# Performance work log

Hardware: AMD Instinct MI355X
Metric: run time of the kernel (lower is better)

## Reference

```python
import jax, jax.numpy as jnp
import numpy as np

B, C, H, W = 8, 64, 128, 128
EPS = 1e-5


def setup_inputs() -> dict:
    key = jax.random.key(0)
    ks = jax.random.split(key, 12)
    d = {
        'x_1': jax.random.normal(ks[0], (B, C, H, W), jnp.float32),
        'x_cur': jax.random.normal(ks[1], (B, C, H, W), jnp.float32),
        # 1x1 conv projections (stored as [out_c, in_c])
        'Wq': jax.random.normal(ks[2], (C, C), jnp.float32) * (1.0 / np.sqrt(C)),
        'bq': jnp.zeros((C,), jnp.float32),
        'Wk': jax.random.normal(ks[3], (C, C), jnp.float32) * (1.0 / np.sqrt(C)),
        'bk': jnp.zeros((C,), jnp.float32),
        'Wv': jax.random.normal(ks[4], (C, C), jnp.float32) * (1.0 / np.sqrt(C)),
        'bv': jnp.zeros((C,), jnp.float32),
        'gamma': jnp.ones((1,), jnp.float32),
        # conv_cur: 3x3 conv (no bias) + BN + ReLU, then 1x1 conv (no bias) + BN + ReLU
        'conv1_w': jax.random.normal(ks[5], (C, C, 3, 3), jnp.float32) * (1.0 / np.sqrt(9 * C)),
        'bn1_scale': jnp.ones((C,), jnp.float32),
        'bn1_bias': jnp.zeros((C,), jnp.float32),
        'bn1_mean': jax.random.normal(ks[6], (C,), jnp.float32) * 0.1,
        'bn1_var': jax.random.uniform(ks[7], (C,), jnp.float32, 0.5, 1.5),
        'conv2_w': jax.random.normal(ks[8], (C, C, 1, 1), jnp.float32) * (1.0 / np.sqrt(C)),
        'bn2_scale': jnp.ones((C,), jnp.float32),
        'bn2_bias': jnp.zeros((C,), jnp.float32),
        'bn2_mean': jax.random.normal(ks[9], (C,), jnp.float32) * 0.1,
        'bn2_var': jax.random.uniform(ks[10], (C,), jnp.float32, 0.5, 1.5),
    }
    return d


def _conv1x1(x, w, b):
    # x: [B,C,H,W], w: [O,C] -> [B,O,H,W]
    return jnp.einsum('oc,bchw->bohw', w, x) + b[None, :, None, None]


def _bn_relu(x, scale, bias, mean, var):
    inv = scale / jnp.sqrt(var + EPS)
    return jax.nn.relu(x * inv[None, :, None, None] + (bias - mean * inv)[None, :, None, None])


def reference(x_1, x_cur, Wq, bq, Wk, bk, Wv, bv, gamma, conv1_w,
              bn1_scale, bn1_bias, bn1_mean, bn1_var, conv2_w,
              bn2_scale, bn2_bias, bn2_mean, bn2_var):
    q = _conv1x1(x_1, Wq, bq)          # [B,C,H,W]
    k = _conv1x1(x_cur, Wk, bk)        # [B,C,H,W]
    v = _conv1x1(x_cur, Wv, bv)        # [B,C,H,W]
    # energy[b,c,w,w'] = sum_h q[b,c,h,w] * k[b,c,h,w']  (Q transposed on H/W)
    energy = jnp.einsum('bchw,bchv->bcwv', q, k)          # [B,C,W,W]
    attention = jax.nn.softmax(energy, axis=2)             # softmax over dim 2
    out = jnp.einsum('bchw,bcwv->bchv', v, attention)      # [B,C,H,W]
    y = gamma * out + x_cur
    # 3x3 conv + BN + ReLU (dropout is identity in eval)
    y = jax.lax.conv_general_dilated(y, conv1_w, (1, 1), 'SAME',
                                     dimension_numbers=('NCHW', 'OIHW', 'NCHW'))
    y = _bn_relu(y, bn1_scale, bn1_bias, bn1_mean, bn1_var)
    # 1x1 conv + BN + ReLU
    y = jnp.einsum('oc,bchw->bohw', conv2_w[:, :, 0, 0], y)
    y = _bn_relu(y, bn2_scale, bn2_bias, bn2_mean, bn2_var)
    return y
```

## Files before the change

kernel.cpp:

```cpp
#include <hip/hip_runtime.h>

#define HW    16384
#define CHW   1048576
#define EPSV  1e-5f
#define PITCH 68
#define APITCH 132

typedef short bf16x8 __attribute__((ext_vector_type(8)));
typedef float f32x4 __attribute__((ext_vector_type(4)));
typedef unsigned short u16x4 __attribute__((ext_vector_type(4)));

static __device__ __forceinline__ unsigned short f2b(float f) {
    union { float f; unsigned int i; } x; x.f = f;
    unsigned int i = x.i + 0x7fffu + ((x.i >> 16) & 1u);
    return (unsigned short)(i >> 16);
}

static __device__ __forceinline__ bf16x8 frag_load(const unsigned short* p) {
    union { u16x4 h[2]; bf16x8 v; } u;
    u.h[0] = *(const u16x4*)(p);
    u.h[1] = *(const u16x4*)(p + 4);
    return u.v;
}
static __device__ __forceinline__ bf16x8 gfrag(const unsigned short* p) {
    return *(const bf16x8*)p;
}
static __device__ __forceinline__ f32x4 mfma16(bf16x8 a, bf16x8 b, f32x4 c) {
    return __builtin_amdgcn_mfma_f32_16x16x32_bf16(a, b, c, 0, 0, 0);
}

__global__ void prep_kernel(const float* __restrict__ Wq, const float* __restrict__ Wk,
                            const float* __restrict__ Wv,
                            const float* __restrict__ c1w,
                            const float* __restrict__ bn1s, const float* __restrict__ bn1b,
                            const float* __restrict__ bn1m, const float* __restrict__ bn1v,
                            const float* __restrict__ c2w,
                            const float* __restrict__ bn2s, const float* __restrict__ bn2b,
                            const float* __restrict__ bn2m, const float* __restrict__ bn2v,
                            unsigned short* __restrict__ Wqb, unsigned short* __restrict__ Wkb,
                            unsigned short* __restrict__ Wvb, unsigned short* __restrict__ W3b,
                            unsigned short* __restrict__ W2b, float* __restrict__ beta1,
                            float* __restrict__ beta2)
{
    int i = blockIdx.x * blockDim.x + threadIdx.x;
    if (i < 12288) {
        int mat = i >> 12, r = i & 4095;
        const float* src = (mat == 0) ? Wq : ((mat == 1) ? Wk : Wv);
        unsigned short* dst = (mat == 0) ? Wqb : ((mat == 1) ? Wkb : Wvb);
        dst[r] = f2b(src[r]);
    } else if (i < 49152) {
        int j = i - 12288;
        int dydx = j >> 12, r = j & 4095, o = r >> 6, c = r & 63;
        float inv = bn1s[o] * rsqrtf(bn1v[o] + EPSV);
        W3b[j] = f2b(c1w[o * 576 + c * 9 + dydx] * inv);
    } else if (i < 53248) {
        int r = i - 49152, o = r >> 6;
        float inv = bn2s[o] * rsqrtf(bn2v[o] + EPSV);
        W2b[r] = f2b(c2w[r] * inv);
    } else if (i < 53376) {
        int j = i - 53248;
        if (j < 64) {
            float inv = bn1s[j] * rsqrtf(bn1v[j] + EPSV);
            beta1[j] = bn1b[j] - bn1m[j] * inv;
        } else {
            int o = j - 64;
            float inv = bn2s[o] * rsqrtf(bn2v[o] + EPSV);
            beta2[o] = bn2b[o] - bn2m[o] * inv;
        }
    }
}

__global__ __launch_bounds__(256) void qkv_kernel(
    const float* __restrict__ x1, const float* __restrict__ xc,
    const unsigned short* __restrict__ Wqb, const unsigned short* __restrict__ Wkb,
    const unsigned short* __restrict__ Wvb,
    const float* __restrict__ bq, const float* __restrict__ bk,
    const float* __restrict__ bv,
    unsigned short* __restrict__ qo, unsigned short* __restrict__ ko,
    unsigned short* __restrict__ vo)
{
    __shared__ __align__(16) unsigned short XT[2][128][PITCH];
    int t = threadIdx.x;
    int b = blockIdx.x >> 7;
    int p0 = (blockIdx.x & 127) << 7;

    const float* xs1 = x1 + b * CHW + p0;
    const float* xs2 = xc + b * CHW + p0;
    for (int idx = t; idx < 2048; idx += 256) {
        int c0 = ((idx >> 6) & 31) << 1, p2 = (idx & 63) << 1;
        float2 a0 = *(const float2*)&xs1[c0 * HW + p2];
        float2 a1 = *(const float2*)&xs1[(c0 + 1) * HW + p2];
        *(unsigned int*)&XT[0][p2][c0]     = f2b(a0.x) | ((unsigned int)f2b(a1.x) << 16);
        *(unsigned int*)&XT[0][p2 + 1][c0] = f2b(a0.y) | ((unsigned int)f2b(a1.y) << 16);
        float2 b0 = *(const float2*)&xs2[c0 * HW + p2];
        float2 b1 = *(const float2*)&xs2[(c0 + 1) * HW + p2];
        *(unsigned int*)&XT[1][p2][c0]     = f2b(b0.x) | ((unsigned int)f2b(b1.x) << 16);
        *(unsigned int*)&XT[1][p2 + 1][c0] = f2b(b0.y) | ((unsigned int)f2b(b1.y) << 16);
    }
    __syncthreads();

    int lane = t & 63, wid = t >> 6;
    int i16 = lane & 15;
    int g8 = (lane >> 4) << 3;
    int g4 = (lane >> 4) << 2;
    int n0 = wid << 5;

    bf16x8 bfr[2][2][2];
    #pragma unroll
    for (int inp = 0; inp < 2; ++inp)
        #pragma unroll
        for (int nt = 0; nt < 2; ++nt)
            #pragma unroll
            for (int ks = 0; ks < 2; ++ks)
                bfr[inp][nt][ks] = frag_load(&XT[inp][n0 + nt * 16 + i16][ks * 32 + g8]);

    f32x4 zz = {0.f, 0.f, 0.f, 0.f};
    f32x4 acc[3][4][2];
    #pragma unroll
    for (int mat = 0; mat < 3; ++mat)
        #pragma unroll
        for (int m = 0; m < 4; ++m) { acc[mat][m][0] = zz; acc[mat][m][1] = zz; }

    #pragma unroll
    for (int mat = 0; mat < 3; ++mat) {
        const unsigned short* Wmat = (mat == 0) ? Wqb : ((mat == 1) ? Wkb : Wvb);
        const int inp = (mat == 0) ? 0 : 1;
        #pragma unroll
        for (int ks = 0; ks < 2; ++ks)
            #pragma unroll
            for (int m = 0; m < 4; ++m) {
                bf16x8 af = gfrag(Wmat + (m * 16 + i16) * 64 + ks * 32 + g8);
                acc[mat][m][0] = mfma16(af, bfr[inp][0][ks], acc[mat][m][0]);
                acc[mat][m][1] = mfma16(af, bfr[inp][1][ks], acc[mat][m][1]);
            }
    }

    #pragma unroll
    for (int mat = 0; mat < 3; ++mat) {
        unsigned short* dst = ((mat == 0) ? qo : ((mat == 1) ? ko : vo)) + b * CHW + p0;
        const float* bias = (mat == 0) ? bq : ((mat == 1) ? bk : bv);
        #pragma unroll
        for (int m = 0; m < 4; ++m)
            #pragma unroll
            for (int r = 0; r < 4; ++r) {
                int o = m * 16 + g4 + r;
                float bb = bias[o];
                dst[o * HW + n0 + i16]      = f2b(acc[mat][m][0][r] + bb);
                dst[o * HW + n0 + 16 + i16] = f2b(acc[mat][m][1][r] + bb);
            }
    }
}

__global__ __launch_bounds__(512) void attn_kernel(
    const unsigned short* __restrict__ q, const unsigned short* __restrict__ k,
    const unsigned short* __restrict__ v, const float* __restrict__ xc,
    const float* __restrict__ gamma_p, unsigned short* __restrict__ y)
{
    extern __shared__ __align__(16) unsigned short sarena[];
    unsigned short (*QT)[APITCH] = (unsigned short(*)[APITCH])sarena;
    unsigned short (*KT)[APITCH] = (unsigned short(*)[APITCH])(sarena + 16896);
    unsigned short (*PL)[APITCH] = QT;

    int t = threadIdx.x;
    int base = blockIdx.x * HW;

    for (int idx = t; idx < 4096; idx += 512) {
        int h0 = (idx >> 6) << 1, w2 = (idx & 63) << 1;
        unsigned int q0 = *(const unsigned int*)&q[base + h0 * 128 + w2];
        unsigned int q1 = *(const unsigned int*)&q[base + (h0 + 1) * 128 + w2];
        *(unsigned int*)&QT[w2][h0]     = (q0 & 0xffffu) | (q1 << 16);
        *(unsigned int*)&QT[w2 + 1][h0] = (q0 >> 16) | (q1 & 0xffff0000u);
        unsigned int k0 = *(const unsigned int*)&k[base + h0 * 128 + w2];
        unsigned int k1 = *(const unsigned int*)&k[base + (h0 + 1) * 128 + w2];
        *(unsigned int*)&KT[w2][h0]     = (k0 & 0xffffu) | (k1 << 16);
        *(unsigned int*)&KT[w2 + 1][h0] = (k0 >> 16) | (k1 & 0xffff0000u);
    }
    __syncthreads();

    int lane = t & 63, wid = t >> 6;
    int i16 = lane & 15;
    int g8 = (lane >> 4) << 3;
    int g4 = (lane >> 4) << 2;
    int m0 = wid << 4;

    f32x4 zz = {0.f, 0.f, 0.f, 0.f};
    f32x4 e[8];
    #pragma unroll
    for (int nt = 0; nt < 8; ++nt) e[nt] = zz;

    #pragma unroll
    for (int ks = 0; ks < 4; ++ks) {
        bf16x8 a0 = frag_load(&KT[m0 + i16][ks * 32 + g8]);
        #pragma unroll
        for (int nt = 0; nt < 8; ++nt) {
            bf16x8 bfq = frag_load(&QT[nt * 16 + i16][ks * 32 + g8]);
            e[nt] = mfma16(a0, bfq, e[nt]);
        }
    }
    __syncthreads();

    #pragma unroll
    for (int r = 0; r < 4; ++r) {
        float mx = e[0][r];
        #pragma unroll
        for (int nt = 1; nt < 8; ++nt) mx = fmaxf(mx, e[nt][r]);
        mx = fmaxf(mx, __shfl_xor(mx, 1));
        mx = fmaxf(mx, __shfl_xor(mx, 2));
        mx = fmaxf(mx, __shfl_xor(mx, 4));
        mx = fmaxf(mx, __shfl_xor(mx, 8));
        float pv[8];
        float s = 0.f;
        #pragma unroll
        for (int nt = 0; nt < 8; ++nt) {
            pv[nt] = __expf(e[nt][r] - mx);
            s += pv[nt];
        }
        s += __shfl_xor(s, 1);
        s += __shfl_xor(s, 2);
        s += __shfl_xor(s, 4);
        s += __shfl_xor(s, 8);
        float rinv = 1.f / s;
        int vr = m0 + g4 + r;
        #pragma unroll
        for (int nt = 0; nt < 8; ++nt)
            PL[vr][nt * 16 + i16] = f2b(pv[nt] * rinv);
    }
    __syncthreads();

    f32x4 o_[8];
    #pragma unroll
    for (int nt = 0; nt < 8; ++nt) o_[nt] = zz;

    const unsigned short* vb_ = v + base;
    #pragma unroll
    for (int ks = 0; ks < 4; ++ks) {
        bf16x8 a0 = gfrag(vb_ + (m0 + i16) * 128 + ks * 32 + g8);
        #pragma unroll
        for (int nt = 0; nt < 8; ++nt) {
            bf16x8 bp = frag_load(&PL[nt * 16 + i16][ks * 32 + g8]);
            o_[nt] = mfma16(a0, bp, o_[nt]);
        }
    }

    float g = gamma_p[0];
    const float* xcb = xc + base;
    #pragma unroll
    for (int nt = 0; nt < 8; ++nt)
        #pragma unroll
        for (int r = 0; r < 4; ++r) {
            int hh = m0 + g4 + r;
            int ww = nt * 16 + i16;
            int idx = hh * 128 + ww;
            y[base + idx] = f2b(fmaf(g, o_[nt][r], xcb[idx]));
        }
}

__global__ __launch_bounds__(512) void conv3_fused_kernel(
    const unsigned short* __restrict__ yin, const unsigned short* __restrict__ W3b,
    const unsigned short* __restrict__ W2b, const float* __restrict__ beta1,
    const float* __restrict__ beta2, float* __restrict__ out)
{
    extern __shared__ __align__(16) unsigned short arena[];
    unsigned short* XT = arena;
    unsigned short* Y2 = arena;

    int t = threadIdx.x;
    int b = blockIdx.x >> 6;
    int h0 = (blockIdx.x & 63) << 1;

    u16x4 z4 = {0, 0, 0, 0};
    if (t < 136) {
        int dy = t / 34, rr = t % 34;
        int row = (rr < 17) ? 0 : 129;
        int q4 = (rr % 17) << 2;
        *(u16x4*)&XT[(dy * 130 + row) * PITCH + q4] = z4;
    }
    const unsigned short* yb = yin + b * CHW;
    for (int idx = t; idx < 8192; idx += 512) {
        int dy = idx >> 11, c0 = ((idx >> 6) & 31) << 1, w2 = (idx & 63) << 1;
        int hh = h0 + dy - 1;
        unsigned int a0 = 0, a1 = 0;
        if (hh >= 0 && hh < 128) {
            a0 = *(const unsigned int*)&yb[c0 * HW + hh * 128 + w2];
            a1 = *(const unsigned int*)&yb[(c0 + 1) * HW + hh * 128 + w2];
        }
        *(unsigned int*)&XT[(dy * 130 + w2 + 1) * PITCH + c0] = (a0 & 0xffffu) | (a1 << 16);
        *(unsigned int*)&XT[(dy * 130 + w2 + 2) * PITCH + c0] = (a0 >> 16) | (a1 & 0xffff0000u);
    }
    __syncthreads();

    int lane = t & 63, wid = t >> 6;
    int i16 = lane & 15;
    int g8 = (lane >> 4) << 3;
    int g4 = (lane >> 4) << 2;
    int orow  = wid >> 2;
    int wbase = ((wid >> 1) & 1) << 6;
    int mbase = (wid & 1) << 1;

    f32x4 zz = {0.f, 0.f, 0.f, 0.f};
    f32x4 acc[2][4];
    #pragma unroll
    for (int m = 0; m < 2; ++m)
        #pragma unroll
        for (int nt = 0; nt < 4; ++nt) acc[m][nt] = zz;

    #pragma unroll
    for (int dy = 0; dy < 3; ++dy)
        #pragma unroll
        for (int dx = 0; dx < 3; ++dx) {
            const unsigned short* wpl = W3b + (dy * 3 + dx) * 4096;
            const unsigned short* xpl = XT + ((dy + orow) * 130 + dx) * PITCH;
            #pragma unroll
            for (int ks = 0; ks < 2; ++ks) {
                bf16x8 bf0 = frag_load(xpl + (wbase + i16) * PITCH + ks * 32 + g8);
                bf16x8 bf1 = frag_load(xpl + (wbase + 16 + i16) * PITCH + ks * 32 + g8);
                bf16x8 bf2 = frag_load(xpl + (wbase + 32 + i16) * PITCH + ks * 32 + g8);
                bf16x8 bf3 = frag_load(xpl + (wbase + 48 + i16) * PITCH + ks * 32 + g8);
                #pragma unroll
                for (int m = 0; m < 2; ++m) {
                    bf16x8 a = gfrag(wpl + ((mbase + m) * 16 + i16) * 64 + ks * 32 + g8);
                    acc[m][0] = mfma16(a, bf0, acc[m][0]);
                    acc[m][1] = mfma16(a, bf1, acc[m][1]);
                    acc[m][2] = mfma16(a, bf2, acc[m][2]);
                    acc[m][3] = mfma16(a, bf3, acc[m][3]);
                }
            }
        }
    __syncthreads();

    #pragma unroll
    for (int m = 0; m < 2; ++m) {
        int ob0 = (mbase + m) * 16 + g4;
        float b0 = beta1[ob0 + 0];
        float b1 = beta1[ob0 + 1];
        float b2 = beta1[ob0 + 2];
        float b3 = beta1[ob0 + 3];
        #pragma unroll
        for (int nt = 0; nt < 4; ++nt) {
            int p = orow * 128 + wbase + nt * 16 + i16;
            u16x4 pk;
            pk[0] = f2b(fmaxf(acc[m][nt][0] + b0, 0.f));
            pk[1] = f2b(fmaxf(acc[m][nt][1] + b1, 0.f));
            pk[2] = f2b(fmaxf(acc[m][nt][2] + b2, 0.f));
            pk[3] = f2b(fmaxf(acc[m][nt][3] + b3, 0.f));
            *(u16x4*)&Y2[p * PITCH + ob0] = pk;
        }
    }
    __syncthreads();

    f32x4 acc2[2][4];
    #pragma unroll
    for (int m = 0; m < 2; ++m)
        #pragma unroll
        for (int nt = 0; nt < 4; ++nt) acc2[m][nt] = zz;

    #pragma unroll
    for (int ks = 0; ks < 2; ++ks) {
        bf16x8 bf0 = frag_load(Y2 + (orow * 128 + wbase + i16) * PITCH + ks * 32 + g8);
        bf16x8 bf1 = frag_load(Y2 + (orow * 128 + wbase + 16 + i16) * PITCH + ks * 32 + g8);
        bf16x8 bf2 = frag_load(Y2 + (orow * 128 + wbase + 32 + i16) * PITCH + ks * 32 + g8);
        bf16x8 bf3 = frag_load(Y2 + (orow * 128 + wbase + 48 + i16) * PITCH + ks * 32 + g8);
        #pragma unroll
        for (int m = 0; m < 2; ++m) {
            bf16x8 a = gfrag(W2b + ((mbase + m) * 16 + i16) * 64 + ks * 32 + g8);
            acc2[m][0] = mfma16(a, bf0, acc2[m][0]);
            acc2[m][1] = mfma16(a, bf1, acc2[m][1]);
            acc2[m][2] = mfma16(a, bf2, acc2[m][2]);
            acc2[m][3] = mfma16(a, bf3, acc2[m][3]);
        }
    }

    float* ob = out + b * CHW + (h0 + orow) * 128 + wbase;
    #pragma unroll
    for (int m = 0; m < 2; ++m)
        #pragma unroll
        for (int r = 0; r < 4; ++r) {
            int o = (mbase + m) * 16 + g4 + r;
            float bt = beta2[o];
            #pragma unroll
            for (int nt = 0; nt < 4; ++nt)
                ob[o * HW + nt * 16 + i16] = fmaxf(acc2[m][nt][r] + bt, 0.f);
        }
}

extern "C" void kernel_launch(void* const* d_in, const int* in_sizes, int n_in,
                              void* d_out, int out_size, void* d_ws, size_t ws_size,
                              hipStream_t stream)
{
    const float* x1   = (const float*)d_in[0];
    const float* xc   = (const float*)d_in[1];
    const float* Wq   = (const float*)d_in[2];
    const float* bq   = (const float*)d_in[3];
    const float* Wk   = (const float*)d_in[4];
    const float* bk   = (const float*)d_in[5];
    const float* Wv   = (const float*)d_in[6];
    const float* bv   = (const float*)d_in[7];
    const float* gam  = (const float*)d_in[8];
    const float* c1w  = (const float*)d_in[9];
    const float* bn1s = (const float*)d_in[10];
    const float* bn1b = (const float*)d_in[11];
    const float* bn1m = (const float*)d_in[12];
    const float* bn1v = (const float*)d_in[13];
    const float* c2w  = (const float*)d_in[14];
    const float* bn2s = (const float*)d_in[15];
    const float* bn2b = (const float*)d_in[16];
    const float* bn2m = (const float*)d_in[17];
    const float* bn2v = (const float*)d_in[18];
    float* out = (float*)d_out;

    char* ws = (char*)d_ws;
    const size_t BUF = 16777216;
    unsigned short* qb  = (unsigned short*)(ws);
    unsigned short* kb  = (unsigned short*)(ws + BUF);
    unsigned short* vb  = (unsigned short*)(ws + 2 * BUF);
    unsigned short* yb  = (unsigned short*)(ws + 3 * BUF);
    unsigned short* Wqb = (unsigned short*)(ws + 4 * BUF);
    unsigned short* Wkb = Wqb + 4096;
    unsigned short* Wvb = Wkb + 4096;
    unsigned short* W3b = Wvb + 4096;
    unsigned short* W2b = W3b + 36864;
    float* beta1 = (float*)(W2b + 4096);
    float* beta2 = beta1 + 64;

    prep_kernel<<<209, 256, 0, stream>>>(Wq, Wk, Wv, c1w, bn1s, bn1b, bn1m, bn1v,
                                         c2w, bn2s, bn2b, bn2m, bn2v,
                                         Wqb, Wkb, Wvb, W3b, W2b, beta1, beta2);
    qkv_kernel<<<1024, 256, 0, stream>>>(x1, xc, Wqb, Wkb, Wvb, bq, bk, bv,
                                         qb, kb, vb);
    hipFuncSetAttribute((const void*)attn_kernel,
                        hipFuncAttributeMaxDynamicSharedMemorySize, 67584);
    attn_kernel<<<512, 512, 67584, stream>>>(qb, kb, vb, xc, gam, yb);
    hipFuncSetAttribute((const void*)conv3_fused_kernel,
                        hipFuncAttributeMaxDynamicSharedMemorySize, 70720);
    conv3_fused_kernel<<<512, 512, 70720, stream>>>(yb, W3b, W2b, beta1, beta2, out);
}
```

Baseline: 217.2 us.

## Vectorize global loads and swap MFMA operands for packed vector stores

Widens the global loads in the qkv, attention and conv staging loops to float4 and 8-element bf16 vectors. In the qkv GEMM, the attention P·V product and the final 1x1 conv, it swaps the MFMA A and B operands so each lane holds four consecutive pixels, which allows packed u16x4 or float4 stores instead of scalar strided writes. In the attention kernel, each wave now reads only its own rows of the probability tile, so one __syncthreads is removed, and the V fragments are read directly from global memory. The aim is to cut the number of memory transactions and a barrier, at the cost of reworked index math and more global traffic for V.

```diff
diff --git a/kernel.cpp b/kernel.cpp
--- a/kernel.cpp
+++ b/kernel.cpp
@@ -9,6 +9,7 @@
 typedef short bf16x8 __attribute__((ext_vector_type(8)));
 typedef float f32x4 __attribute__((ext_vector_type(4)));
 typedef unsigned short u16x4 __attribute__((ext_vector_type(4)));
+typedef unsigned short u16x8 __attribute__((ext_vector_type(8)));
 
 static __device__ __forceinline__ unsigned short f2b(float f) {
     union { float f; unsigned int i; } x; x.f = f;
@@ -86,16 +87,20 @@
 
     const float* xs1 = x1 + b * CHW + p0;
     const float* xs2 = xc + b * CHW + p0;
-    for (int idx = t; idx < 2048; idx += 256) {
-        int c0 = ((idx >> 6) & 31) << 1, p2 = (idx & 63) << 1;
-        float2 a0 = *(const float2*)&xs1[c0 * HW + p2];
-        float2 a1 = *(const float2*)&xs1[(c0 + 1) * HW + p2];
-        *(unsigned int*)&XT[0][p2][c0]     = f2b(a0.x) | ((unsigned int)f2b(a1.x) << 16);
-        *(unsigned int*)&XT[0][p2 + 1][c0] = f2b(a0.y) | ((unsigned int)f2b(a1.y) << 16);
-        float2 b0 = *(const float2*)&xs2[c0 * HW + p2];
-        float2 b1 = *(const float2*)&xs2[(c0 + 1) * HW + p2];
-        *(unsigned int*)&XT[1][p2][c0]     = f2b(b0.x) | ((unsigned int)f2b(b1.x) << 16);
-        *(unsigned int*)&XT[1][p2 + 1][c0] = f2b(b0.y) | ((unsigned int)f2b(b1.y) << 16);
+    for (int idx = t; idx < 1024; idx += 256) {
+        int c0 = ((idx >> 5) & 31) << 1, p4 = (idx & 31) << 2;
+        float4 a0 = *(const float4*)&xs1[c0 * HW + p4];
+        float4 a1 = *(const float4*)&xs1[(c0 + 1) * HW + p4];
+        *(unsigned int*)&XT[0][p4 + 0][c0] = f2b(a0.x) | ((unsigned int)f2b(a1.x) << 16);
+        *(unsigned int*)&XT[0][p4 + 1][c0] = f2b(a0.y) | ((unsigned int)f2b(a1.y) << 16);
+        *(unsigned int*)&XT[0][p4 + 2][c0] = f2b(a0.z) | ((unsigned int)f2b(a1.z) << 16);
+        *(unsigned int*)&XT[0][p4 + 3][c0] = f2b(a0.w) | ((unsigned int)f2b(a1.w) << 16);
+        float4 b0 = *(const float4*)&xs2[c0 * HW + p4];
+        float4 b1 = *(const float4*)&xs2[(c0 + 1) * HW + p4];
+        *(unsigned int*)&XT[1][p4 + 0][c0] = f2b(b0.x) | ((unsigned int)f2b(b1.x) << 16);
+        *(unsigned int*)&XT[1][p4 + 1][c0] = f2b(b0.y) | ((unsigned int)f2b(b1.y) << 16);
+        *(unsigned int*)&XT[1][p4 + 2][c0] = f2b(b0.z) | ((unsigned int)f2b(b1.z) << 16);
+        *(unsigned int*)&XT[1][p4 + 3][c0] = f2b(b0.w) | ((unsigned int)f2b(b1.w) << 16);
     }
     __syncthreads();
 
@@ -103,51 +108,54 @@
     int i16 = lane & 15;
     int g8 = (lane >> 4) << 3;
     int g4 = (lane >> 4) << 2;
-    int n0 = wid << 5;
-
-    bf16x8 bfr[2][2][2];
+    int pb = wid << 5;
+
+    bf16x8 afr[2][2][2];
     #pragma unroll
     for (int inp = 0; inp < 2; ++inp)
         #pragma unroll
-        for (int nt = 0; nt < 2; ++nt)
+        for (int mi = 0; mi < 2; ++mi)
             #pragma unroll
             for (int ks = 0; ks < 2; ++ks)
-                bfr[inp][nt][ks] = frag_load(&XT[inp][n0 + nt * 16 + i16][ks * 32 + g8]);
+                afr[inp][mi][ks] = frag_load(&XT[inp][pb + mi * 16 + i16][ks * 32 + g8]);
 
     f32x4 zz = {0.f, 0.f, 0.f, 0.f};
-    f32x4 acc[3][4][2];
-    #pragma unroll
-    for (int mat = 0; mat < 3; ++mat)
-        #pragma unroll
-        for (int m = 0; m < 4; ++m) { acc[mat][m][0] = zz; acc[mat][m][1] = zz; }
-
     #pragma unroll
     for (int mat = 0; mat < 3; ++mat) {
         const unsigned short* Wmat = (mat == 0) ? Wqb : ((mat == 1) ? Wkb : Wvb);
+        unsigned short* dst = ((mat == 0) ? qo : ((mat == 1) ? ko : vo)) + b * CHW + p0;
+        const float* bias = (mat == 0) ? bq : ((mat == 1) ? bk : bv);
         const int inp = (mat == 0) ? 0 : 1;
+
+        f32x4 acc[2][4];
+        #pragma unroll
+        for (int mi = 0; mi < 2; ++mi)
+            #pragma unroll
+            for (int nt = 0; nt < 4; ++nt) acc[mi][nt] = zz;
+
         #pragma unroll
         for (int ks = 0; ks < 2; ++ks)
             #pragma unroll
-            for (int m = 0; m < 4; ++m) {
-                bf16x8 af = gfrag(Wmat + (m * 16 + i16) * 64 + ks * 32 + g8);
-                acc[mat][m][0] = mfma16(af, bfr[inp][0][ks], acc[mat][m][0]);
-                acc[mat][m][1] = mfma16(af, bfr[inp][1][ks], acc[mat][m][1]);
+            for (int nt = 0; nt < 4; ++nt) {
+                bf16x8 bw = gfrag(Wmat + (nt * 16 + i16) * 64 + ks * 32 + g8);
+                acc[0][nt] = mfma16(afr[inp][0][ks], bw, acc[0][nt]);
+                acc[1][nt] = mfma16(afr[inp][1][ks], bw, acc[1][nt]);
             }
-    }
-
-    #pragma unroll
-    for (int mat = 0; mat < 3; ++mat) {
-        unsigned short* dst = ((mat == 0) ? qo : ((mat == 1) ? ko : vo)) + b * CHW + p0;
-        const float* bias = (mat == 0) ? bq : ((mat == 1) ? bk : bv);
-        #pragma unroll
-        for (int m = 0; m < 4; ++m)
+
+        #pragma unroll
+        for (int nt = 0; nt < 4; ++nt) {
+            int o = nt * 16 + i16;
+            float bb = bias[o];
             #pragma unroll
-            for (int r = 0; r < 4; ++r) {
-                int o = m * 16 + g4 + r;
-                float bb = bias[o];
-                dst[o * HW + n0 + i16]      = f2b(acc[mat][m][0][r] + bb);
-                dst[o * HW + n0 + 16 + i16] = f2b(acc[mat][m][1][r] + bb);
+            for (int mi = 0; mi < 2; ++mi) {
+                u16x4 pk;
+                pk[0] = f2b(acc[mi][nt][0] + bb);
+                pk[1] = f2b(acc[mi][nt][1] + bb);
+                pk[2] = f2b(acc[mi][nt][2] + bb);
+                pk[3] = f2b(acc[mi][nt][3] + bb);
+                *(u16x4*)&dst[o * HW + pb + mi * 16 + g4] = pk;
             }
+        }
     }
 }
 
@@ -164,16 +172,18 @@
     int t = threadIdx.x;
     int base = blockIdx.x * HW;
 
-    for (int idx = t; idx < 4096; idx += 512) {
-        int h0 = (idx >> 6) << 1, w2 = (idx & 63) << 1;
-        unsigned int q0 = *(const unsigned int*)&q[base + h0 * 128 + w2];
-        unsigned int q1 = *(const unsigned int*)&q[base + (h0 + 1) * 128 + w2];
-        *(unsigned int*)&QT[w2][h0]     = (q0 & 0xffffu) | (q1 << 16);
-        *(unsigned int*)&QT[w2 + 1][h0] = (q0 >> 16) | (q1 & 0xffff0000u);
-        unsigned int k0 = *(const unsigned int*)&k[base + h0 * 128 + w2];
-        unsigned int k1 = *(const unsigned int*)&k[base + (h0 + 1) * 128 + w2];
-        *(unsigned int*)&KT[w2][h0]     = (k0 & 0xffffu) | (k1 << 16);
-        *(unsigned int*)&KT[w2 + 1][h0] = (k0 >> 16) | (k1 & 0xffff0000u);
+    for (int idx = t; idx < 1024; idx += 512) {
+        int h0 = (idx >> 4) << 1, w8 = (idx & 15) << 3;
+        u16x8 q0 = *(const u16x8*)&q[base + h0 * 128 + w8];
+        u16x8 q1 = *(const u16x8*)&q[base + (h0 + 1) * 128 + w8];
+        #pragma unroll
+        for (int j = 0; j < 8; ++j)
+            *(unsigned int*)&QT[w8 + j][h0] = (unsigned int)q0[j] | ((unsigned int)q1[j] << 16);
+        u16x8 k0 = *(const u16x8*)&k[base + h0 * 128 + w8];
+        u16x8 k1 = *(const u16x8*)&k[base + (h0 + 1) * 128 + w8];
+        #pragma unroll
+        for (int j = 0; j < 8; ++j)
+            *(unsigned int*)&KT[w8 + j][h0] = (unsigned int)k0[j] | ((unsigned int)k1[j] << 16);
     }
     __syncthreads();
 
@@ -225,34 +235,39 @@
         for (int nt = 0; nt < 8; ++nt)
             PL[vr][nt * 16 + i16] = f2b(pv[nt] * rinv);
     }
-    __syncthreads();
 
     f32x4 o_[8];
     #pragma unroll
     for (int nt = 0; nt < 8; ++nt) o_[nt] = zz;
 
+    bf16x8 ap[4];
+    #pragma unroll
+    for (int ks = 0; ks < 4; ++ks)
+        ap[ks] = frag_load(&PL[m0 + i16][ks * 32 + g8]);
+
     const unsigned short* vb_ = v + base;
     #pragma unroll
-    for (int ks = 0; ks < 4; ++ks) {
-        bf16x8 a0 = gfrag(vb_ + (m0 + i16) * 128 + ks * 32 + g8);
+    for (int ks = 0; ks < 4; ++ks)
         #pragma unroll
         for (int nt = 0; nt < 8; ++nt) {
-            bf16x8 bp = frag_load(&PL[nt * 16 + i16][ks * 32 + g8]);
-            o_[nt] = mfma16(a0, bp, o_[nt]);
-        }
-    }
+            bf16x8 bv8 = gfrag(vb_ + (nt * 16 + i16) * 128 + ks * 32 + g8);
+            o_[nt] = mfma16(ap[ks], bv8, o_[nt]);
+        }
 
     float g = gamma_p[0];
     const float* xcb = xc + base;
     #pragma unroll
-    for (int nt = 0; nt < 8; ++nt)
-        #pragma unroll
-        for (int r = 0; r < 4; ++r) {
-            int hh = m0 + g4 + r;
-            int ww = nt * 16 + i16;
-            int idx = hh * 128 + ww;
-            y[base + idx] = f2b(fmaf(g, o_[nt][r], xcb[idx]));
-        }
+    for (int nt = 0; nt < 8; ++nt) {
+        int hh = nt * 16 + i16;
+        int v4 = m0 + g4;
+        float4 xcv = *(const float4*)&xcb[hh * 128 + v4];
+        u16x4 pk;
+        pk[0] = f2b(fmaf(g, o_[nt][0], xcv.x));
+        pk[1] = f2b(fmaf(g, o_[nt][1], xcv.y));
+        pk[2] = f2b(fmaf(g, o_[nt][2], xcv.z));
+        pk[3] = f2b(fmaf(g, o_[nt][3], xcv.w));
+        *(u16x4*)&y[base + hh * 128 + v4] = pk;
+    }
 }
 
 __global__ __launch_bounds__(512) void conv3_fused_kernel(
@@ -276,16 +291,18 @@
         *(u16x4*)&XT[(dy * 130 + row) * PITCH + q4] = z4;
     }
     const unsigned short* yb = yin + b * CHW;
-    for (int idx = t; idx < 8192; idx += 512) {
-        int dy = idx >> 11, c0 = ((idx >> 6) & 31) << 1, w2 = (idx & 63) << 1;
+    for (int idx = t; idx < 2048; idx += 512) {
+        int dy = idx >> 9, c0 = ((idx >> 4) & 31) << 1, w8 = (idx & 15) << 3;
         int hh = h0 + dy - 1;
-        unsigned int a0 = 0, a1 = 0;
+        u16x8 a0 = {0,0,0,0,0,0,0,0}, a1 = {0,0,0,0,0,0,0,0};
         if (hh >= 0 && hh < 128) {
-            a0 = *(const unsigned int*)&yb[c0 * HW + hh * 128 + w2];
-            a1 = *(const unsigned int*)&yb[(c0 + 1) * HW + hh * 128 + w2];
-        }
-        *(unsigned int*)&XT[(dy * 130 + w2 + 1) * PITCH + c0] = (a0 & 0xffffu) | (a1 << 16);
-        *(unsigned int*)&XT[(dy * 130 + w2 + 2) * PITCH + c0] = (a0 >> 16) | (a1 & 0xffff0000u);
+            a0 = *(const u16x8*)&yb[c0 * HW + hh * 128 + w8];
+            a1 = *(const u16x8*)&yb[(c0 + 1) * HW + hh * 128 + w8];
+        }
+        #pragma unroll
+        for (int j = 0; j < 8; ++j)
+            *(unsigned int*)&XT[(dy * 130 + w8 + 1 + j) * PITCH + c0] =
+                (unsigned int)a0[j] | ((unsigned int)a1[j] << 16);
     }
     __syncthreads();
 
@@ -348,6 +365,7 @@
     }
     __syncthreads();
 
+    int m0c = wid << 5;
     f32x4 acc2[2][4];
     #pragma unroll
     for (int m = 0; m < 2; ++m)
@@ -356,30 +374,31 @@
 
     #pragma unroll
     for (int ks = 0; ks < 2; ++ks) {
-        bf16x8 bf0 = frag_load(Y2 + (orow * 128 + wbase + i16) * PITCH + ks * 32 + g8);
-        bf16x8 bf1 = frag_load(Y2 + (orow * 128 + wbase + 16 + i16) * PITCH + ks * 32 + g8);
-        bf16x8 bf2 = frag_load(Y2 + (orow * 128 + wbase + 32 + i16) * PITCH + ks * 32 + g8);
-        bf16x8 bf3 = frag_load(Y2 + (orow * 128 + wbase + 48 + i16) * PITCH + ks * 32 + g8);
-        #pragma unroll
-        for (int m = 0; m < 2; ++m) {
-            bf16x8 a = gfrag(W2b + ((mbase + m) * 16 + i16) * 64 + ks * 32 + g8);
-            acc2[m][0] = mfma16(a, bf0, acc2[m][0]);
-            acc2[m][1] = mfma16(a, bf1, acc2[m][1]);
-            acc2[m][2] = mfma16(a, bf2, acc2[m][2]);
-            acc2[m][3] = mfma16(a, bf3, acc2[m][3]);
-        }
-    }
-
-    float* ob = out + b * CHW + (h0 + orow) * 128 + wbase;
-    #pragma unroll
-    for (int m = 0; m < 2; ++m)
-        #pragma unroll
-        for (int r = 0; r < 4; ++r) {
-            int o = (mbase + m) * 16 + g4 + r;
-            float bt = beta2[o];
-            #pragma unroll
-            for (int nt = 0; nt < 4; ++nt)
-                ob[o * HW + nt * 16 + i16] = fmaxf(acc2[m][nt][r] + bt, 0.f);
+        bf16x8 ay0 = frag_load(Y2 + (m0c + i16) * PITCH + ks * 32 + g8);
+        bf16x8 ay1 = frag_load(Y2 + (m0c + 16 + i16) * PITCH + ks * 32 + g8);
+        #pragma unroll
+        for (int nt = 0; nt < 4; ++nt) {
+            bf16x8 bw = gfrag(W2b + (nt * 16 + i16) * 64 + ks * 32 + g8);
+            acc2[0][nt] = mfma16(ay0, bw, acc2[0][nt]);
+            acc2[1][nt] = mfma16(ay1, bw, acc2[1][nt]);
+        }
+    }
+
+    float* ob = out + b * CHW;
+    #pragma unroll
+    for (int mi = 0; mi < 2; ++mi)
+        #pragma unroll
+        for (int nt = 0; nt < 4; ++nt) {
+            int o2 = nt * 16 + i16;
+            float bt = beta2[o2];
+            int p = m0c + mi * 16 + g4;
+            int orw = p >> 7, wl = p & 127;
+            float4 vv;
+            vv.x = fmaxf(acc2[mi][nt][0] + bt, 0.f);
+            vv.y = fmaxf(acc2[mi][nt][1] + bt, 0.f);
+            vv.z = fmaxf(acc2[mi][nt][2] + bt, 0.f);
+            vv.w = fmaxf(acc2[mi][nt][3] + bt, 0.f);
+            *(float4*)&ob[o2 * HW + (h0 + orw) * 128 + wl] = vv;
         }
 }
 
```

New measurement: 211.8 us. 1.03x faster.
